# Performance work log

Hardware: AMD Instinct MI355X
Metric: run time of the kernel (lower is better)

Reference implementation:

```python
import jax, jax.numpy as jnp
import numpy as np

B, T, S, C, E, H = 4, 2048, 2048, 256, 512, 8
D = E // H
SCALE = E ** (-0.5)


def setup_inputs() -> dict:
    key = jax.random.key(0)
    ks = jax.random.split(key, 12)
    x = jax.random.normal(ks[0], (B, T, C), dtype=jnp.float32)
    context = jax.random.normal(ks[1], (B, S, E), dtype=jnp.float32)
    pad_mask = jax.random.randint(ks[2], (B, T, S), 0, 2) == 1
    p = 0.02
    # Conv1d kernel_size=1 weights stored squeezed: [out_ch, in_ch]
    w_in = jax.random.normal(ks[3], (E, C), dtype=jnp.float32) * p
    b_in = jnp.zeros((E,), dtype=jnp.float32)
    wq = jax.random.normal(ks[4], (E, E), dtype=jnp.float32) * p
    bq = jnp.zeros((E,), dtype=jnp.float32)
    wk = jax.random.normal(ks[5], (E, E), dtype=jnp.float32) * p
    bk = jnp.zeros((E,), dtype=jnp.float32)
    wv = jax.random.normal(ks[6], (E, E), dtype=jnp.float32) * p
    bv = jnp.zeros((E,), dtype=jnp.float32)
    w_out = jax.random.normal(ks[7], (C, E), dtype=jnp.float32) * p
    b_out = jnp.zeros((C,), dtype=jnp.float32)
    return {"x": x, "context": context, "pad_mask": pad_mask,
            "w_in": w_in, "b_in": b_in, "wq": wq, "bq": bq,
            "wk": wk, "bk": bk, "wv": wv, "bv": bv,
            "w_out": w_out, "b_out": b_out}


def reference(x, context, pad_mask, w_in, b_in, wq, bq, wk, bk, wv, bv, w_out, b_out):
    # proj_in: Conv1d k=1 == per-token linear on channel dim. [B,T,C] -> [B,T,E]
    xe = jnp.einsum('btc,ec->bte', x, w_in) + b_in
    Q = (xe @ wq.T + bq).reshape(B, T, H, D)       # query tokens
    K = (context @ wk.T + bk).reshape(B, S, H, D)  # key tokens
    V = (context @ wv.T + bv).reshape(B, S, H, D)
    att = jnp.einsum('bihd,bjhd->bhij', Q, K) * SCALE  # [B,H,T,S]
    att = jnp.where(pad_mask[:, None, :, :], jnp.float32(-1e9), att)
    att = jax.nn.softmax(att, axis=-1)
    out = jnp.einsum('bhij,bjhd->bihd', att, V).reshape(B, T, E)
    # proj_out: Conv1d k=1, [B,T,E] -> [B,T,C]
    out = jnp.einsum('bte,ce->btc', out, w_out) + b_out
    return out
```

## Files before the change

kernel.cpp:

```cpp
#include <hip/hip_runtime.h>
#include <cstdint>
#include <cstddef>

#define Bb 4
#define Tt 2048
#define Ssz 2048
#define Cc 256
#define Ee 512
#define Hh 8
#define LDK 1024

typedef short bf8 __attribute__((ext_vector_type(8)));
typedef float f4 __attribute__((ext_vector_type(4)));

__device__ __forceinline__ unsigned short f2bf(float x) {
  unsigned int u = __float_as_uint(x);
  u += 0x7fffu + ((u >> 16) & 1u);
  return (unsigned short)(u >> 16);
}

__global__ __launch_bounds__(256) void castk(const float* __restrict__ s,
                                             unsigned short* __restrict__ d,
                                             int n4) {
  int i = blockIdx.x * 256 + threadIdx.x;
  if (i < n4) {
    float4 v = ((const float4*)s)[i];
    ushort4 o;
    o.x = f2bf(v.x);
    o.y = f2bf(v.y);
    o.z = f2bf(v.z);
    o.w = f2bf(v.w);
    ((ushort4*)d)[i] = o;
  }
}

__global__ __launch_bounds__(256) void castw(const float* __restrict__ w0, const float* __restrict__ w1,
                                             const float* __restrict__ w2, const float* __restrict__ w3,
                                             unsigned short* __restrict__ o0, unsigned short* __restrict__ o1,
                                             unsigned short* __restrict__ o2, unsigned short* __restrict__ o3,
                                             float qsc) {
  int i = blockIdx.x * 256 + threadIdx.x;
  const float* s;
  unsigned short* d;
  int off;
  float sc = 1.f;
  if (i < 65536)       { s = w0; d = o0; off = i; sc = qsc; }
  else if (i < 131072) { s = w1; d = o1; off = i - 65536; }
  else if (i < 196608) { s = w2; d = o2; off = i - 131072; }
  else                 { s = w3; d = o3; off = i - 196608; }
  float4 v = ((const float4*)s)[off];
  ushort4 o;
  o.x = f2bf(v.x * sc);
  o.y = f2bf(v.y * sc);
  o.z = f2bf(v.z * sc);
  o.w = f2bf(v.w * sc);
  ((ushort4*)d)[off] = o;
}

__global__ __launch_bounds__(256) void tcast(const float* __restrict__ w,
                                             unsigned short* __restrict__ o) {
  __shared__ float t[64][65];
  const int c0 = blockIdx.x * 64, e0 = blockIdx.y * 64;
  const int tid = threadIdx.x;
  const int row = tid >> 2, c4 = (tid & 3) * 4;
#pragma unroll
  for (int l = 0; l < 4; l++) {
    float4 v = *(const float4*)(w + (size_t)(e0 + row) * Cc + c0 + c4 + l * 16);
    t[row][c4 + l * 16 + 0] = v.x;
    t[row][c4 + l * 16 + 1] = v.y;
    t[row][c4 + l * 16 + 2] = v.z;
    t[row][c4 + l * 16 + 3] = v.w;
  }
  __syncthreads();
#pragma unroll
  for (int l = 0; l < 2; l++) {
    int id = tid + l * 256;
    int c = id >> 3, ch = id & 7;
    bf8 ov;
#pragma unroll
    for (int k = 0; k < 8; k++) {
      int kk = (k + c) & 7;
      ov[kk] = (short)f2bf(t[ch * 8 + kk][c]);
    }
    *(bf8*)(o + (size_t)(c0 + c) * Ee + e0 + ch * 8) = ov;
  }
}

__global__ __launch_bounds__(256) void bqin_k(const float* __restrict__ wq,
                                              const float* __restrict__ b_in,
                                              const float* __restrict__ bq,
                                              float* __restrict__ out, float qsc) {
  int i = blockIdx.x * 256 + threadIdx.x;
  float s = 0.f;
  for (int e = 0; e < Ee; e += 4) {
    float4 w = *(const float4*)(wq + (size_t)i * Ee + e);
    float4 b = *(const float4*)(b_in + e);
    s += w.x * b.x + w.y * b.y + w.z * b.z + w.w * b.w;
  }
  out[i] = (s + bq[i]) * qsc;
}

__global__ __launch_bounds__(256) void packmask(const int* __restrict__ m,
                                                unsigned int* __restrict__ p, int nwords) {
  int i = blockIdx.x * 256 + threadIdx.x;
  if (i >= nwords) return;
  const int4* src = (const int4*)m + (size_t)i * 8;
  unsigned int w = 0;
#pragma unroll
  for (int k = 0; k < 8; k++) {
    int4 v = src[k];
    w |= (unsigned int)(v.x != 0) << (k * 4);
    w |= (unsigned int)(v.y != 0) << (k * 4 + 1);
    w |= (unsigned int)(v.z != 0) << (k * 4 + 2);
    w |= (unsigned int)(v.w != 0) << (k * 4 + 3);
  }
  p[i] = w;
}

__global__ __launch_bounds__(256) void vtrans(const unsigned short* __restrict__ V, int ldv,
                                              unsigned short* __restrict__ Vt) {
  __shared__ unsigned short tile[64][72];
  const int tid = threadIdx.x;
  const int b = blockIdx.z, h = blockIdx.y, s0 = blockIdx.x * 64;
#pragma unroll
  for (int i = 0; i < 2; i++) {
    int id = tid + i * 256;
    int row = id >> 3, c = id & 7;
    *(bf8*)&tile[row][c * 8] =
        *(const bf8*)(V + (size_t)(b * Ssz + s0 + row) * ldv + h * 64 + c * 8);
  }
  __syncthreads();
#pragma unroll
  for (int i = 0; i < 2; i++) {
    int id = tid + i * 256;
    int d = id >> 3, c = id & 7;
    bf8 o;
#pragma unroll
    for (int k = 0; k < 8; k++) {
      int kk = (k + d) & 7;
      o[kk] = (short)tile[c * 8 + kk][d];
    }
    *(bf8*)(Vt + (size_t)((b * Hh + h) * 64 + d) * Ssz + s0 + c * 8) = o;
  }
}

template <bool OUT_BF16, int BM, int BN, int WGM>
__global__ __launch_bounds__(256) void gemm_bt(const unsigned short* __restrict__ A,
                                               const unsigned short* __restrict__ Bt,
                                               const float* __restrict__ bias0,
                                               const float* __restrict__ bias1, int split,
                                               void* __restrict__ Cout,
                                               int M, int N, int K) {
  constexpr int WGN = 4 / WGM;
  constexpr int MI = BM / (WGM * 16);
  constexpr int NJ = BN / (WGN * 16);
  constexpr int NA = BM / 32;
  constexpr int NB = BN / 32;
  __shared__ unsigned short As[BM][72];
  __shared__ unsigned short Bs[BN][72];
  const int tid = threadIdx.x;
  const int wave = tid >> 6, lane = tid & 63;
  const int lrow = lane & 15, quad = lane >> 4;
  const int wm = (wave / WGN) * (BM / WGM);
  const int wn = (wave % WGN) * (BN / WGN);
  const int m0 = blockIdx.x * BM, n0 = blockIdx.y * BN;
  const int arow = tid >> 3, ac = tid & 7;

  f4 acc[MI][NJ];
#pragma unroll
  for (int i = 0; i < MI; i++)
#pragma unroll
    for (int j = 0; j < NJ; j++) {
      f4 z = {0.f, 0.f, 0.f, 0.f};
      acc[i][j] = z;
    }

  bf8 apre[NA], bpre[NB];
#pragma unroll
  for (int i = 0; i < NA; i++)
    apre[i] = *(const bf8*)(A + (size_t)(m0 + arow + i * 32) * K + ac * 8);
#pragma unroll
  for (int i = 0; i < NB; i++)
    bpre[i] = *(const bf8*)(Bt + (size_t)(n0 + arow + i * 32) * K + ac * 8);

  const int nkt = K >> 6;
  for (int kt = 0; kt < nkt; ++kt) {
#pragma unroll
    for (int i = 0; i < NA; i++) *(bf8*)&As[arow + i * 32][ac * 8] = apre[i];
#pragma unroll
    for (int i = 0; i < NB; i++) *(bf8*)&Bs[arow + i * 32][ac * 8] = bpre[i];
    __syncthreads();
    if (kt + 1 < nkt) {
      int k0 = (kt + 1) << 6;
#pragma unroll
      for (int i = 0; i < NA; i++)
        apre[i] = *(const bf8*)(A + (size_t)(m0 + arow + i * 32) * K + k0 + ac * 8);
#pragma unroll
      for (int i = 0; i < NB; i++)
        bpre[i] = *(const bf8*)(Bt + (size_t)(n0 + arow + i * 32) * K + k0 + ac * 8);
    }
#pragma unroll
    for (int kk = 0; kk < 2; kk++) {
      bf8 af[MI], bff[NJ];
#pragma unroll
      for (int i = 0; i < MI; i++)
        af[i] = *(const bf8*)&As[wm + i * 16 + lrow][kk * 32 + quad * 8];
#pragma unroll
      for (int j = 0; j < NJ; j++)
        bff[j] = *(const bf8*)&Bs[wn + j * 16 + lrow][kk * 32 + quad * 8];
#pragma unroll
      for (int i = 0; i < MI; i++)
#pragma unroll
        for (int j = 0; j < NJ; j++)
          acc[i][j] = __builtin_amdgcn_mfma_f32_16x16x32_bf16(af[i], bff[j],
                                                              acc[i][j], 0, 0, 0);
    }
    __syncthreads();
  }

#pragma unroll
  for (int j = 0; j < NJ; j++) {
    int col = n0 + wn + j * 16 + lrow;
    float bvv = 0.f;
    if (bias0) bvv = (col < split) ? bias0[col] : bias1[col - split];
#pragma unroll
    for (int i = 0; i < MI; i++) {
#pragma unroll
      for (int r = 0; r < 4; r++) {
        int row = m0 + wm + i * 16 + quad * 4 + r;
        float v = acc[i][j][r] + bvv;
        if (OUT_BF16)
          ((unsigned short*)Cout)[(size_t)row * N + col] = f2bf(v);
        else
          ((float*)Cout)[(size_t)row * N + col] = v;
      }
    }
  }
}

__global__ __launch_bounds__(256) void attn(const unsigned short* __restrict__ Q,
                                            const unsigned short* __restrict__ K,
                                            const unsigned short* __restrict__ Vt,
                                            const unsigned int* __restrict__ mp,
                                            unsigned short* __restrict__ O) {
  __shared__ unsigned short Ks[64][72];
  __shared__ unsigned short Vts[64][72];
  __shared__ unsigned short Ps[128][72];
  const int tid = threadIdx.x;
  const int wave = tid >> 6, lane = tid & 63;
  const int lrow = lane & 15, quad = lane >> 4;
  const int b = blockIdx.z, h = blockIdx.y, t0 = blockIdx.x * 128;
  const int arow = tid >> 3, ac = tid & 7;
  const int wm = wave * 32;

#pragma unroll
  for (int i = 0; i < 4; i++) {
    int row = arow + i * 32;
    *(bf8*)&Ps[row][ac * 8] =
        *(const bf8*)(Q + (size_t)(b * Tt + t0 + row) * Ee + h * 64 + ac * 8);
  }
  __syncthreads();
  bf8 qf[2][2];
#pragma unroll
  for (int mi = 0; mi < 2; mi++) {
    qf[mi][0] = *(const bf8*)&Ps[wm + mi * 16 + lrow][quad * 8];
    qf[mi][1] = *(const bf8*)&Ps[wm + mi * 16 + lrow][32 + quad * 8];
  }

  f4 oacc[2][4];
  f4 dacc[2];
#pragma unroll
  for (int mi = 0; mi < 2; mi++) {
    f4 z = {0.f, 0.f, 0.f, 0.f};
    dacc[mi] = z;
#pragma unroll
    for (int j = 0; j < 4; j++) oacc[mi][j] = z;
  }
  bf8 ones;
#pragma unroll
  for (int k = 0; k < 8; k++) ones[k] = (short)0x3F80;

  const unsigned short* Kbase = K + (size_t)b * Ssz * LDK + h * 64;
  const unsigned short* Vbase = Vt + (size_t)((b * Hh + h) * 64) * Ssz;

  bf8 kreg[2], vreg[2];
#pragma unroll
  for (int i = 0; i < 2; i++) {
    int row = arow + i * 32;
    kreg[i] = *(const bf8*)(Kbase + (size_t)row * LDK + ac * 8);
    vreg[i] = *(const bf8*)(Vbase + (size_t)row * Ssz + ac * 8);
  }

  for (int s0 = 0; s0 < Ssz; s0 += 64) {
    __syncthreads();
#pragma unroll
    for (int i = 0; i < 2; i++) {
      int row = arow + i * 32;
      *(bf8*)&Ks[row][ac * 8] = kreg[i];
      *(bf8*)&Vts[row][ac * 8] = vreg[i];
    }
    __syncthreads();
    if (s0 + 64 < Ssz) {
#pragma unroll
      for (int i = 0; i < 2; i++) {
        int row = arow + i * 32;
        kreg[i] = *(const bf8*)(Kbase + (size_t)(s0 + 64 + row) * LDK + ac * 8);
        vreg[i] = *(const bf8*)(Vbase + (size_t)row * Ssz + s0 + 64 + ac * 8);
      }
    }
    uint2 mw[2][4];
#pragma unroll
    for (int mi = 0; mi < 2; mi++)
#pragma unroll
      for (int r = 0; r < 4; r++)
        mw[mi][r] = *(const uint2*)(mp + (size_t)(b * Tt + t0 + wm + mi * 16 + quad * 4 + r) * 64 +
                                    (s0 >> 5));

#pragma unroll
    for (int j = 0; j < 4; j++) {
      bf8 kf0 = *(const bf8*)&Ks[j * 16 + lrow][quad * 8];
      bf8 kf1 = *(const bf8*)&Ks[j * 16 + lrow][32 + quad * 8];
      f4 s[2];
      f4 z = {0.f, 0.f, 0.f, 0.f};
      s[0] = z; s[1] = z;
      s[0] = __builtin_amdgcn_mfma_f32_16x16x32_bf16(qf[0][0], kf0, s[0], 0, 0, 0);
      s[0] = __builtin_amdgcn_mfma_f32_16x16x32_bf16(qf[0][1], kf1, s[0], 0, 0, 0);
      s[1] = __builtin_amdgcn_mfma_f32_16x16x32_bf16(qf[1][0], kf0, s[1], 0, 0, 0);
      s[1] = __builtin_amdgcn_mfma_f32_16x16x32_bf16(qf[1][1], kf1, s[1], 0, 0, 0);
      const int col = j * 16 + lrow;
      const unsigned int bit = ((j & 1) << 4) + lrow;
#pragma unroll
      for (int mi = 0; mi < 2; mi++) {
#pragma unroll
        for (int r = 0; r < 4; r++) {
          unsigned int w = (j >> 1) ? mw[mi][r].y : mw[mi][r].x;
          float e = __builtin_amdgcn_exp2f(s[mi][r]);
          float p = ((w >> bit) & 1u) ? 0.f : e;
          Ps[wm + mi * 16 + quad * 4 + r][col] =
              (unsigned short)(__float_as_uint(p) >> 16);
        }
      }
    }
#pragma unroll
    for (int kk = 0; kk < 2; kk++) {
      bf8 pf[2];
#pragma unroll
      for (int mi = 0; mi < 2; mi++) {
        pf[mi] = *(const bf8*)&Ps[wm + mi * 16 + lrow][kk * 32 + quad * 8];
        dacc[mi] = __builtin_amdgcn_mfma_f32_16x16x32_bf16(pf[mi], ones, dacc[mi], 0, 0, 0);
      }
#pragma unroll
      for (int j = 0; j < 4; j++) {
        bf8 vf = *(const bf8*)&Vts[j * 16 + lrow][kk * 32 + quad * 8];
#pragma unroll
        for (int mi = 0; mi < 2; mi++)
          oacc[mi][j] = __builtin_amdgcn_mfma_f32_16x16x32_bf16(pf[mi], vf, oacc[mi][j], 0, 0, 0);
      }
    }
  }

#pragma unroll
  for (int mi = 0; mi < 2; mi++) {
#pragma unroll
    for (int r = 0; r < 4; r++) {
      float inv = 1.0f / dacc[mi][r];
      int row = b * Tt + t0 + wm + mi * 16 + quad * 4 + r;
#pragma unroll
      for (int j = 0; j < 4; j++)
        O[(size_t)row * Ee + h * 64 + j * 16 + lrow] = f2bf(oacc[mi][j][r] * inv);
    }
  }
}

extern "C" void kernel_launch(void* const* d_in, const int* in_sizes, int n_in,
                              void* d_out, int out_size, void* d_ws, size_t ws_size,
                              hipStream_t stream) {
  const float* x    = (const float*)d_in[0];
  const float* ctx  = (const float*)d_in[1];
  const int*   mask = (const int*)d_in[2];
  const float* w_in = (const float*)d_in[3];
  const float* b_in = (const float*)d_in[4];
  const float* wq   = (const float*)d_in[5];
  const float* bq   = (const float*)d_in[6];
  const float* wk   = (const float*)d_in[7];
  const float* bk   = (const float*)d_in[8];
  const float* wv   = (const float*)d_in[9];
  const float* bv   = (const float*)d_in[10];
  const float* wo   = (const float*)d_in[11];
  const float* bo   = (const float*)d_in[12];

  const float qsc = 0.04419417382415922f * 1.4426950408889634f;

  unsigned short* ws = (unsigned short*)d_ws;
  unsigned short* xb   = ws;
  unsigned short* cb   = ws + 2097152;
  unsigned short* wqb  = ws + 6291456;
  unsigned short* wkb  = ws + 6553600;
  unsigned short* wvb  = ws + 6815744;
  unsigned short* wob  = ws + 7077888;
  unsigned short* Qb   = ws + 7208960;
  unsigned short* KVb  = ws + 11403264;
  unsigned short* Ob   = ws + 19791872;
  unsigned short* wqin = Ob;
  unsigned short* winT = Ob + 131072;
  float*          bqinb = (float*)(Ob + 262144);
  unsigned int*   maskp = (unsigned int*)xb;
  unsigned short* Vtb  = cb;

  castk<<<2048, 256, 0, stream>>>(x, xb, 524288);
  castk<<<4096, 256, 0, stream>>>(ctx, cb, 1048576);
  castw<<<896, 256, 0, stream>>>(wq, wk, wv, wo, wqb, wkb, wvb, wob, qsc);
  tcast<<<dim3(4, 8), 256, 0, stream>>>(w_in, winT);
  bqin_k<<<2, 256, 0, stream>>>(wq, b_in, bq, bqinb, qsc);

  gemm_bt<true, 64, 64, 2><<<dim3(8, 4), 256, 0, stream>>>(
      wqb, winT, nullptr, nullptr, 256, wqin, 512, 256, 512);
  gemm_bt<true, 128, 64, 2><<<dim3(64, 8), 256, 0, stream>>>(
      xb, wqin, bqinb, nullptr, 512, Qb, 8192, 512, 256);
  packmask<<<2048, 256, 0, stream>>>(mask, maskp, 524288);
  gemm_bt<true, 128, 128, 2><<<dim3(64, 8), 256, 0, stream>>>(
      cb, wkb, bk, bv, 512, KVb, 8192, 1024, 512);
  vtrans<<<dim3(32, 8, 4), 256, 0, stream>>>(KVb + 512, LDK, Vtb);

  attn<<<dim3(16, 8, 4), 256, 0, stream>>>(Qb, KVb, Vtb, maskp, Ob);

  gemm_bt<false, 64, 64, 2><<<dim3(128, 4), 256, 0, stream>>>(
      Ob, wob, bo, nullptr, 256, d_out, 8192, 256, 512);
}
```

Baseline: 275.2 us.

## Fuse prep kernels, merge mask packing into KV GEMM, double-buffer attention tiles

The separate cast, transpose, bias and weight-product kernels are merged into one multi-role `prep` launch, which now computes wq·w_in straight from fp32 inputs. Mask packing shares a launch with the K/V projection GEMM. The GEMM body is factored into a reusable device function. In attention, K/V shared tiles are double-buffered so one barrier per iteration can be dropped. The score MFMA operands are swapped so each lane's mask word per row is loaded once and P is written as packed ushort4. The aim is fewer launches, fewer barriers and fewer mask loads and LDS stores, at the cost of more shared memory in attention and heterogeneous block roles.

```diff
diff --git a/kernel.cpp b/kernel.cpp
--- a/kernel.cpp
+++ b/kernel.cpp
@@ -19,128 +19,96 @@
   return (unsigned short)(u >> 16);
 }
 
-__global__ __launch_bounds__(256) void castk(const float* __restrict__ s,
-                                             unsigned short* __restrict__ d,
-                                             int n4) {
-  int i = blockIdx.x * 256 + threadIdx.x;
-  if (i < n4) {
-    float4 v = ((const float4*)s)[i];
-    ushort4 o;
-    o.x = f2bf(v.x);
-    o.y = f2bf(v.y);
-    o.z = f2bf(v.z);
-    o.w = f2bf(v.w);
-    ((ushort4*)d)[i] = o;
-  }
-}
-
-__global__ __launch_bounds__(256) void castw(const float* __restrict__ w0, const float* __restrict__ w1,
-                                             const float* __restrict__ w2, const float* __restrict__ w3,
-                                             unsigned short* __restrict__ o0, unsigned short* __restrict__ o1,
-                                             unsigned short* __restrict__ o2, unsigned short* __restrict__ o3,
-                                             float qsc) {
-  int i = blockIdx.x * 256 + threadIdx.x;
-  const float* s;
-  unsigned short* d;
-  int off;
-  float sc = 1.f;
-  if (i < 65536)       { s = w0; d = o0; off = i; sc = qsc; }
-  else if (i < 131072) { s = w1; d = o1; off = i - 65536; }
-  else if (i < 196608) { s = w2; d = o2; off = i - 131072; }
-  else                 { s = w3; d = o3; off = i - 196608; }
-  float4 v = ((const float4*)s)[off];
-  ushort4 o;
-  o.x = f2bf(v.x * sc);
-  o.y = f2bf(v.y * sc);
-  o.z = f2bf(v.z * sc);
-  o.w = f2bf(v.w * sc);
-  ((ushort4*)d)[off] = o;
-}
-
-__global__ __launch_bounds__(256) void tcast(const float* __restrict__ w,
-                                             unsigned short* __restrict__ o) {
-  __shared__ float t[64][65];
-  const int c0 = blockIdx.x * 64, e0 = blockIdx.y * 64;
+template <bool OUT_BF16, int BM, int BN, int WGM>
+__device__ __forceinline__ void gemm_core(unsigned short (*As)[72],
+                                          unsigned short (*Bs)[72],
+                                          const unsigned short* __restrict__ A,
+                                          const unsigned short* __restrict__ Bt,
+                                          const float* __restrict__ bias0,
+                                          const float* __restrict__ bias1, int split,
+                                          void* __restrict__ Cout,
+                                          int M, int N, int K, int m0, int n0) {
+  constexpr int WGN = 4 / WGM;
+  constexpr int MI = BM / (WGM * 16);
+  constexpr int NJ = BN / (WGN * 16);
+  constexpr int NA = BM / 32;
+  constexpr int NB = BN / 32;
   const int tid = threadIdx.x;
-  const int row = tid >> 2, c4 = (tid & 3) * 4;
-#pragma unroll
-  for (int l = 0; l < 4; l++) {
-    float4 v = *(const float4*)(w + (size_t)(e0 + row) * Cc + c0 + c4 + l * 16);
-    t[row][c4 + l * 16 + 0] = v.x;
-    t[row][c4 + l * 16 + 1] = v.y;
-    t[row][c4 + l * 16 + 2] = v.z;
-    t[row][c4 + l * 16 + 3] = v.w;
-  }
-  __syncthreads();
-#pragma unroll
-  for (int l = 0; l < 2; l++) {
-    int id = tid + l * 256;
-    int c = id >> 3, ch = id & 7;
-    bf8 ov;
-#pragma unroll
-    for (int k = 0; k < 8; k++) {
-      int kk = (k + c) & 7;
-      ov[kk] = (short)f2bf(t[ch * 8 + kk][c]);
-    }
-    *(bf8*)(o + (size_t)(c0 + c) * Ee + e0 + ch * 8) = ov;
-  }
-}
-
-__global__ __launch_bounds__(256) void bqin_k(const float* __restrict__ wq,
-                                              const float* __restrict__ b_in,
-                                              const float* __restrict__ bq,
-                                              float* __restrict__ out, float qsc) {
-  int i = blockIdx.x * 256 + threadIdx.x;
-  float s = 0.f;
-  for (int e = 0; e < Ee; e += 4) {
-    float4 w = *(const float4*)(wq + (size_t)i * Ee + e);
-    float4 b = *(const float4*)(b_in + e);
-    s += w.x * b.x + w.y * b.y + w.z * b.z + w.w * b.w;
-  }
-  out[i] = (s + bq[i]) * qsc;
-}
-
-__global__ __launch_bounds__(256) void packmask(const int* __restrict__ m,
-                                                unsigned int* __restrict__ p, int nwords) {
-  int i = blockIdx.x * 256 + threadIdx.x;
-  if (i >= nwords) return;
-  const int4* src = (const int4*)m + (size_t)i * 8;
-  unsigned int w = 0;
-#pragma unroll
-  for (int k = 0; k < 8; k++) {
-    int4 v = src[k];
-    w |= (unsigned int)(v.x != 0) << (k * 4);
-    w |= (unsigned int)(v.y != 0) << (k * 4 + 1);
-    w |= (unsigned int)(v.z != 0) << (k * 4 + 2);
-    w |= (unsigned int)(v.w != 0) << (k * 4 + 3);
-  }
-  p[i] = w;
-}
-
-__global__ __launch_bounds__(256) void vtrans(const unsigned short* __restrict__ V, int ldv,
-                                              unsigned short* __restrict__ Vt) {
-  __shared__ unsigned short tile[64][72];
-  const int tid = threadIdx.x;
-  const int b = blockIdx.z, h = blockIdx.y, s0 = blockIdx.x * 64;
-#pragma unroll
-  for (int i = 0; i < 2; i++) {
-    int id = tid + i * 256;
-    int row = id >> 3, c = id & 7;
-    *(bf8*)&tile[row][c * 8] =
-        *(const bf8*)(V + (size_t)(b * Ssz + s0 + row) * ldv + h * 64 + c * 8);
-  }
-  __syncthreads();
-#pragma unroll
-  for (int i = 0; i < 2; i++) {
-    int id = tid + i * 256;
-    int d = id >> 3, c = id & 7;
-    bf8 o;
-#pragma unroll
-    for (int k = 0; k < 8; k++) {
-      int kk = (k + d) & 7;
-      o[kk] = (short)tile[c * 8 + kk][d];
-    }
-    *(bf8*)(Vt + (size_t)((b * Hh + h) * 64 + d) * Ssz + s0 + c * 8) = o;
+  const int wave = tid >> 6, lane = tid & 63;
+  const int lrow = lane & 15, quad = lane >> 4;
+  const int wm = (wave / WGN) * (BM / WGM);
+  const int wn = (wave % WGN) * (BN / WGN);
+  const int arow = tid >> 3, ac = tid & 7;
+
+  f4 acc[MI][NJ];
+#pragma unroll
+  for (int i = 0; i < MI; i++)
+#pragma unroll
+    for (int j = 0; j < NJ; j++) {
+      f4 z = {0.f, 0.f, 0.f, 0.f};
+      acc[i][j] = z;
+    }
+
+  bf8 apre[NA], bpre[NB];
+#pragma unroll
+  for (int i = 0; i < NA; i++)
+    apre[i] = *(const bf8*)(A + (size_t)(m0 + arow + i * 32) * K + ac * 8);
+#pragma unroll
+  for (int i = 0; i < NB; i++)
+    bpre[i] = *(const bf8*)(Bt + (size_t)(n0 + arow + i * 32) * K + ac * 8);
+
+  const int nkt = K >> 6;
+  for (int kt = 0; kt < nkt; ++kt) {
+#pragma unroll
+    for (int i = 0; i < NA; i++) *(bf8*)&As[arow + i * 32][ac * 8] = apre[i];
+#pragma unroll
+    for (int i = 0; i < NB; i++) *(bf8*)&Bs[arow + i * 32][ac * 8] = bpre[i];
+    __syncthreads();
+    if (kt + 1 < nkt) {
+      int k0 = (kt + 1) << 6;
+#pragma unroll
+      for (int i = 0; i < NA; i++)
+        apre[i] = *(const bf8*)(A + (size_t)(m0 + arow + i * 32) * K + k0 + ac * 8);
+#pragma unroll
+      for (int i = 0; i < NB; i++)
+        bpre[i] = *(const bf8*)(Bt + (size_t)(n0 + arow + i * 32) * K + k0 + ac * 8);
+    }
+#pragma unroll
+    for (int kk = 0; kk < 2; kk++) {
+      bf8 af[MI], bff[NJ];
+#pragma unroll
+      for (int i = 0; i < MI; i++)
+        af[i] = *(const bf8*)&As[wm + i * 16 + lrow][kk * 32 + quad * 8];
+#pragma unroll
+      for (int j = 0; j < NJ; j++)
+        bff[j] = *(const bf8*)&Bs[wn + j * 16 + lrow][kk * 32 + quad * 8];
+#pragma unroll
+      for (int i = 0; i < MI; i++)
+#pragma unroll
+        for (int j = 0; j < NJ; j++)
+          acc[i][j] = __builtin_amdgcn_mfma_f32_16x16x32_bf16(af[i], bff[j],
+                                                              acc[i][j], 0, 0, 0);
+    }
+    __syncthreads();
+  }
+
+#pragma unroll
+  for (int j = 0; j < NJ; j++) {
+    int col = n0 + wn + j * 16 + lrow;
+    float bvv = 0.f;
+    if (bias0) bvv = (col < split) ? bias0[col] : bias1[col - split];
+#pragma unroll
+    for (int i = 0; i < MI; i++) {
+#pragma unroll
+      for (int r = 0; r < 4; r++) {
+        int row = m0 + wm + i * 16 + quad * 4 + r;
+        float v = acc[i][j][r] + bvv;
+        if (OUT_BF16)
+          ((unsigned short*)Cout)[(size_t)row * N + col] = f2bf(v);
+        else
+          ((float*)Cout)[(size_t)row * N + col] = v;
+      }
+    }
   }
 }
 
@@ -151,90 +119,181 @@
                                                const float* __restrict__ bias1, int split,
                                                void* __restrict__ Cout,
                                                int M, int N, int K) {
-  constexpr int WGN = 4 / WGM;
-  constexpr int MI = BM / (WGM * 16);
-  constexpr int NJ = BN / (WGN * 16);
-  constexpr int NA = BM / 32;
-  constexpr int NB = BN / 32;
   __shared__ unsigned short As[BM][72];
   __shared__ unsigned short Bs[BN][72];
+  gemm_core<OUT_BF16, BM, BN, WGM>(As, Bs, A, Bt, bias0, bias1, split, Cout, M, N, K,
+                                   blockIdx.x * BM, blockIdx.y * BN);
+}
+
+__global__ __launch_bounds__(256) void prep(const float* __restrict__ x,
+                                            const float* __restrict__ ctx,
+                                            const float* __restrict__ w_in,
+                                            const float* __restrict__ b_in,
+                                            const float* __restrict__ wq,
+                                            const float* __restrict__ bq,
+                                            const float* __restrict__ wk,
+                                            const float* __restrict__ wv,
+                                            const float* __restrict__ wo,
+                                            unsigned short* __restrict__ xb,
+                                            unsigned short* __restrict__ cb,
+                                            unsigned short* __restrict__ wkvb,
+                                            unsigned short* __restrict__ wob,
+                                            unsigned short* __restrict__ wqin,
+                                            float* __restrict__ bqinb, float qsc) {
+  __shared__ unsigned short sh[128][72];
+  const int bid = blockIdx.x, tid = threadIdx.x;
+  if (bid < 6144) {
+    const float* s;
+    unsigned short* d;
+    int i;
+    if (bid < 2048) { s = x; d = xb; i = bid * 256 + tid; }
+    else            { s = ctx; d = cb; i = (bid - 2048) * 256 + tid; }
+    float4 v = ((const float4*)s)[i];
+    ushort4 o;
+    o.x = f2bf(v.x); o.y = f2bf(v.y); o.z = f2bf(v.z); o.w = f2bf(v.w);
+    ((ushort4*)d)[i] = o;
+  } else if (bid < 6784) {
+    int i = (bid - 6144) * 256 + tid;
+    const float* s;
+    unsigned short* d;
+    int off;
+    if (i < 131072)      { s = wk; d = wkvb; off = i; }
+    else                 { s = wo; d = wob; off = i - 131072; }
+    if (i >= 65536 && i < 131072) { s = wv; off = i - 65536; d = wkvb + 262144; }
+    float4 v = ((const float4*)s)[off];
+    ushort4 o;
+    o.x = f2bf(v.x); o.y = f2bf(v.y); o.z = f2bf(v.z); o.w = f2bf(v.w);
+    ((ushort4*)d)[off] = o;
+  } else if (bid < 6816) {
+    const int idx = bid - 6784;
+    const int m0 = (idx & 7) * 64, n0 = (idx >> 3) * 64;
+    unsigned short (*As)[72] = (unsigned short (*)[72]) & sh[0][0];
+    unsigned short (*Bs)[72] = (unsigned short (*)[72]) & sh[64][0];
+    const int wave = tid >> 6, lane = tid & 63;
+    const int lrow = lane & 15, quad = lane >> 4;
+    const int wm = (wave >> 1) * 32, wn = (wave & 1) * 32;
+    const int arow = tid >> 3, ac = tid & 7;
+    f4 acc[2][2];
+#pragma unroll
+    for (int i = 0; i < 2; i++)
+#pragma unroll
+      for (int j = 0; j < 2; j++) {
+        f4 z = {0.f, 0.f, 0.f, 0.f};
+        acc[i][j] = z;
+      }
+    for (int kt = 0; kt < 8; kt++) {
+#pragma unroll
+      for (int i = 0; i < 2; i++) {
+        int row = arow + i * 32;
+        const float* src = wq + (size_t)(m0 + row) * Ee + kt * 64 + ac * 8;
+        float4 v0 = *(const float4*)src, v1 = *(const float4*)(src + 4);
+        bf8 av;
+        av[0] = (short)f2bf(v0.x * qsc); av[1] = (short)f2bf(v0.y * qsc);
+        av[2] = (short)f2bf(v0.z * qsc); av[3] = (short)f2bf(v0.w * qsc);
+        av[4] = (short)f2bf(v1.x * qsc); av[5] = (short)f2bf(v1.y * qsc);
+        av[6] = (short)f2bf(v1.z * qsc); av[7] = (short)f2bf(v1.w * qsc);
+        *(bf8*)&As[row][ac * 8] = av;
+        int c = n0 + row;
+        bf8 bv;
+#pragma unroll
+        for (int k = 0; k < 8; k++)
+          bv[k] = (short)f2bf(w_in[(size_t)(kt * 64 + ac * 8 + k) * Cc + c]);
+        *(bf8*)&Bs[row][ac * 8] = bv;
+      }
+      __syncthreads();
+#pragma unroll
+      for (int kk = 0; kk < 2; kk++) {
+        bf8 af[2], bff[2];
+#pragma unroll
+        for (int i = 0; i < 2; i++) af[i] = *(const bf8*)&As[wm + i * 16 + lrow][kk * 32 + quad * 8];
+#pragma unroll
+        for (int j = 0; j < 2; j++) bff[j] = *(const bf8*)&Bs[wn + j * 16 + lrow][kk * 32 + quad * 8];
+#pragma unroll
+        for (int i = 0; i < 2; i++)
+#pragma unroll
+          for (int j = 0; j < 2; j++)
+            acc[i][j] = __builtin_amdgcn_mfma_f32_16x16x32_bf16(af[i], bff[j], acc[i][j], 0, 0, 0);
+      }
+      __syncthreads();
+    }
+#pragma unroll
+    for (int j = 0; j < 2; j++)
+#pragma unroll
+      for (int i = 0; i < 2; i++)
+#pragma unroll
+        for (int r = 0; r < 4; r++)
+          wqin[(size_t)(m0 + wm + i * 16 + quad * 4 + r) * Cc + n0 + wn + j * 16 + lrow] =
+              f2bf(acc[i][j][r]);
+  } else {
+    const int o = (bid - 6816) * 32 + (tid >> 3);
+    const int k0 = (tid & 7) * 64;
+    float s = 0.f;
+#pragma unroll
+    for (int i = 0; i < 16; i++) {
+      float4 w = *(const float4*)(wq + (size_t)o * Ee + k0 + i * 4);
+      float4 bb = *(const float4*)(b_in + k0 + i * 4);
+      s += w.x * bb.x + w.y * bb.y + w.z * bb.z + w.w * bb.w;
+    }
+    s += __shfl_xor(s, 1);
+    s += __shfl_xor(s, 2);
+    s += __shfl_xor(s, 4);
+    if ((tid & 7) == 0) bqinb[o] = (s + bq[o]) * qsc;
+  }
+}
+
+__global__ __launch_bounds__(256) void kvpack(const unsigned short* __restrict__ cb,
+                                              const unsigned short* __restrict__ wkv,
+                                              const float* __restrict__ bk,
+                                              const float* __restrict__ bv,
+                                              unsigned short* __restrict__ KVout,
+                                              const int* __restrict__ mask,
+                                              unsigned int* __restrict__ mp) {
+  __shared__ unsigned short As[128][72];
+  __shared__ unsigned short Bs[128][72];
+  const int bid = blockIdx.x;
+  if (bid < 512) {
+    gemm_core<true, 128, 128, 2>(As, Bs, cb, wkv, bk, bv, 512, KVout, 8192, 1024, 512,
+                                 (bid & 63) * 128, (bid >> 6) * 128);
+  } else {
+    int i = (bid - 512) * 256 + threadIdx.x;
+    const int4* src = (const int4*)mask + (size_t)i * 8;
+    unsigned int w = 0;
+#pragma unroll
+    for (int k = 0; k < 8; k++) {
+      int4 v = src[k];
+      w |= (unsigned int)(v.x != 0) << (k * 4);
+      w |= (unsigned int)(v.y != 0) << (k * 4 + 1);
+      w |= (unsigned int)(v.z != 0) << (k * 4 + 2);
+      w |= (unsigned int)(v.w != 0) << (k * 4 + 3);
+    }
+    mp[i] = w;
+  }
+}
+
+__global__ __launch_bounds__(256) void vtrans(const unsigned short* __restrict__ V, int ldv,
+                                              unsigned short* __restrict__ Vt) {
+  __shared__ unsigned short tile[64][72];
   const int tid = threadIdx.x;
-  const int wave = tid >> 6, lane = tid & 63;
-  const int lrow = lane & 15, quad = lane >> 4;
-  const int wm = (wave / WGN) * (BM / WGM);
-  const int wn = (wave % WGN) * (BN / WGN);
-  const int m0 = blockIdx.x * BM, n0 = blockIdx.y * BN;
-  const int arow = tid >> 3, ac = tid & 7;
-
-  f4 acc[MI][NJ];
-#pragma unroll
-  for (int i = 0; i < MI; i++)
-#pragma unroll
-    for (int j = 0; j < NJ; j++) {
-      f4 z = {0.f, 0.f, 0.f, 0.f};
-      acc[i][j] = z;
-    }
-
-  bf8 apre[NA], bpre[NB];
-#pragma unroll
-  for (int i = 0; i < NA; i++)
-    apre[i] = *(const bf8*)(A + (size_t)(m0 + arow + i * 32) * K + ac * 8);
-#pragma unroll
-  for (int i = 0; i < NB; i++)
-    bpre[i] = *(const bf8*)(Bt + (size_t)(n0 + arow + i * 32) * K + ac * 8);
-
-  const int nkt = K >> 6;
-  for (int kt = 0; kt < nkt; ++kt) {
-#pragma unroll
-    for (int i = 0; i < NA; i++) *(bf8*)&As[arow + i * 32][ac * 8] = apre[i];
-#pragma unroll
-    for (int i = 0; i < NB; i++) *(bf8*)&Bs[arow + i * 32][ac * 8] = bpre[i];
-    __syncthreads();
-    if (kt + 1 < nkt) {
-      int k0 = (kt + 1) << 6;
-#pragma unroll
-      for (int i = 0; i < NA; i++)
-        apre[i] = *(const bf8*)(A + (size_t)(m0 + arow + i * 32) * K + k0 + ac * 8);
-#pragma unroll
-      for (int i = 0; i < NB; i++)
-        bpre[i] = *(const bf8*)(Bt + (size_t)(n0 + arow + i * 32) * K + k0 + ac * 8);
-    }
-#pragma unroll
-    for (int kk = 0; kk < 2; kk++) {
-      bf8 af[MI], bff[NJ];
-#pragma unroll
-      for (int i = 0; i < MI; i++)
-        af[i] = *(const bf8*)&As[wm + i * 16 + lrow][kk * 32 + quad * 8];
-#pragma unroll
-      for (int j = 0; j < NJ; j++)
-        bff[j] = *(const bf8*)&Bs[wn + j * 16 + lrow][kk * 32 + quad * 8];
-#pragma unroll
-      for (int i = 0; i < MI; i++)
-#pragma unroll
-        for (int j = 0; j < NJ; j++)
-          acc[i][j] = __builtin_amdgcn_mfma_f32_16x16x32_bf16(af[i], bff[j],
-                                                              acc[i][j], 0, 0, 0);
-    }
-    __syncthreads();
-  }
-
-#pragma unroll
-  for (int j = 0; j < NJ; j++) {
-    int col = n0 + wn + j * 16 + lrow;
-    float bvv = 0.f;
-    if (bias0) bvv = (col < split) ? bias0[col] : bias1[col - split];
-#pragma unroll
-    for (int i = 0; i < MI; i++) {
-#pragma unroll
-      for (int r = 0; r < 4; r++) {
-        int row = m0 + wm + i * 16 + quad * 4 + r;
-        float v = acc[i][j][r] + bvv;
-        if (OUT_BF16)
-          ((unsigned short*)Cout)[(size_t)row * N + col] = f2bf(v);
-        else
-          ((float*)Cout)[(size_t)row * N + col] = v;
-      }
-    }
+  const int b = blockIdx.z, h = blockIdx.y, s0 = blockIdx.x * 64;
+#pragma unroll
+  for (int i = 0; i < 2; i++) {
+    int id = tid + i * 256;
+    int row = id >> 3, c = id & 7;
+    *(bf8*)&tile[row][c * 8] =
+        *(const bf8*)(V + (size_t)(b * Ssz + s0 + row) * ldv + h * 64 + c * 8);
+  }
+  __syncthreads();
+#pragma unroll
+  for (int i = 0; i < 2; i++) {
+    int id = tid + i * 256;
+    int d = id >> 3, c = id & 7;
+    bf8 o;
+#pragma unroll
+    for (int k = 0; k < 8; k++) {
+      int kk = (k + d) & 7;
+      o[kk] = (short)tile[c * 8 + kk][d];
+    }
+    *(bf8*)(Vt + (size_t)((b * Hh + h) * 64 + d) * Ssz + s0 + c * 8) = o;
   }
 }
 
@@ -243,8 +302,8 @@
                                             const unsigned short* __restrict__ Vt,
                                             const unsigned int* __restrict__ mp,
                                             unsigned short* __restrict__ O) {
-  __shared__ unsigned short Ks[64][72];
-  __shared__ unsigned short Vts[64][72];
+  __shared__ unsigned short Ks[2][64][72];
+  __shared__ unsigned short Vts[2][64][72];
   __shared__ unsigned short Ps[128][72];
   const int tid = threadIdx.x;
   const int wave = tid >> 6, lane = tid & 63;
@@ -282,6 +341,8 @@
 
   const unsigned short* Kbase = K + (size_t)b * Ssz * LDK + h * 64;
   const unsigned short* Vbase = Vt + (size_t)((b * Hh + h) * 64) * Ssz;
+  const unsigned int* mrow0 = mp + (size_t)(b * Tt + t0 + wm + lrow) * 64;
+  const unsigned int* mrow1 = mp + (size_t)(b * Tt + t0 + wm + 16 + lrow) * 64;
 
   bf8 kreg[2], vreg[2];
 #pragma unroll
@@ -291,13 +352,13 @@
     vreg[i] = *(const bf8*)(Vbase + (size_t)row * Ssz + ac * 8);
   }
 
+  int buf = 0;
   for (int s0 = 0; s0 < Ssz; s0 += 64) {
-    __syncthreads();
 #pragma unroll
     for (int i = 0; i < 2; i++) {
       int row = arow + i * 32;
-      *(bf8*)&Ks[row][ac * 8] = kreg[i];
-      *(bf8*)&Vts[row][ac * 8] = vreg[i];
+      *(bf8*)&Ks[buf][row][ac * 8] = kreg[i];
+      *(bf8*)&Vts[buf][row][ac * 8] = vreg[i];
     }
     __syncthreads();
     if (s0 + 64 < Ssz) {
@@ -308,37 +369,37 @@
         vreg[i] = *(const bf8*)(Vbase + (size_t)row * Ssz + s0 + 64 + ac * 8);
       }
     }
-    uint2 mw[2][4];
-#pragma unroll
-    for (int mi = 0; mi < 2; mi++)
-#pragma unroll
-      for (int r = 0; r < 4; r++)
-        mw[mi][r] = *(const uint2*)(mp + (size_t)(b * Tt + t0 + wm + mi * 16 + quad * 4 + r) * 64 +
-                                    (s0 >> 5));
-
-#pragma unroll
-    for (int j = 0; j < 4; j++) {
-      bf8 kf0 = *(const bf8*)&Ks[j * 16 + lrow][quad * 8];
-      bf8 kf1 = *(const bf8*)&Ks[j * 16 + lrow][32 + quad * 8];
-      f4 s[2];
+    const uint2 mw0 = *(const uint2*)(mrow0 + (s0 >> 5));
+    const uint2 mw1 = *(const uint2*)(mrow1 + (s0 >> 5));
+
+#pragma unroll
+    for (int sf = 0; sf < 4; sf++) {
+      bf8 kf0 = *(const bf8*)&Ks[buf][sf * 16 + lrow][quad * 8];
+      bf8 kf1 = *(const bf8*)&Ks[buf][sf * 16 + lrow][32 + quad * 8];
+      f4 sa[2];
       f4 z = {0.f, 0.f, 0.f, 0.f};
-      s[0] = z; s[1] = z;
-      s[0] = __builtin_amdgcn_mfma_f32_16x16x32_bf16(qf[0][0], kf0, s[0], 0, 0, 0);
-      s[0] = __builtin_amdgcn_mfma_f32_16x16x32_bf16(qf[0][1], kf1, s[0], 0, 0, 0);
-      s[1] = __builtin_amdgcn_mfma_f32_16x16x32_bf16(qf[1][0], kf0, s[1], 0, 0, 0);
-      s[1] = __builtin_amdgcn_mfma_f32_16x16x32_bf16(qf[1][1], kf1, s[1], 0, 0, 0);
-      const int col = j * 16 + lrow;
-      const unsigned int bit = ((j & 1) << 4) + lrow;
+      sa[0] = z; sa[1] = z;
+      sa[0] = __builtin_amdgcn_mfma_f32_16x16x32_bf16(kf0, qf[0][0], sa[0], 0, 0, 0);
+      sa[0] = __builtin_amdgcn_mfma_f32_16x16x32_bf16(kf1, qf[0][1], sa[0], 0, 0, 0);
+      sa[1] = __builtin_amdgcn_mfma_f32_16x16x32_bf16(kf0, qf[1][0], sa[1], 0, 0, 0);
+      sa[1] = __builtin_amdgcn_mfma_f32_16x16x32_bf16(kf1, qf[1][1], sa[1], 0, 0, 0);
 #pragma unroll
       for (int mi = 0; mi < 2; mi++) {
+        const uint2 mw = mi ? mw1 : mw0;
+        const unsigned int w = (sf >= 2) ? mw.y : mw.x;
+        ushort4 pk;
 #pragma unroll
         for (int r = 0; r < 4; r++) {
-          unsigned int w = (j >> 1) ? mw[mi][r].y : mw[mi][r].x;
-          float e = __builtin_amdgcn_exp2f(s[mi][r]);
+          const unsigned int bit = (sf & 1) * 16 + quad * 4 + r;
+          float e = __builtin_amdgcn_exp2f(sa[mi][r]);
           float p = ((w >> bit) & 1u) ? 0.f : e;
-          Ps[wm + mi * 16 + quad * 4 + r][col] =
-              (unsigned short)(__float_as_uint(p) >> 16);
+          unsigned short pb = (unsigned short)(__float_as_uint(p) >> 16);
+          if (r == 0) pk.x = pb;
+          else if (r == 1) pk.y = pb;
+          else if (r == 2) pk.z = pb;
+          else pk.w = pb;
         }
+        *(ushort4*)&Ps[wm + mi * 16 + lrow][sf * 16 + quad * 4] = pk;
       }
     }
 #pragma unroll
@@ -351,12 +412,13 @@
       }
 #pragma unroll
       for (int j = 0; j < 4; j++) {
-        bf8 vf = *(const bf8*)&Vts[j * 16 + lrow][kk * 32 + quad * 8];
+        bf8 vf = *(const bf8*)&Vts[buf][j * 16 + lrow][kk * 32 + quad * 8];
 #pragma unroll
         for (int mi = 0; mi < 2; mi++)
           oacc[mi][j] = __builtin_amdgcn_mfma_f32_16x16x32_bf16(pf[mi], vf, oacc[mi][j], 0, 0, 0);
       }
     }
+    buf ^= 1;
   }
 
 #pragma unroll
@@ -392,38 +454,25 @@
   const float qsc = 0.04419417382415922f * 1.4426950408889634f;
 
   unsigned short* ws = (unsigned short*)d_ws;
-  unsigned short* xb   = ws;
-  unsigned short* cb   = ws + 2097152;
-  unsigned short* wqb  = ws + 6291456;
-  unsigned short* wkb  = ws + 6553600;
-  unsigned short* wvb  = ws + 6815744;
-  unsigned short* wob  = ws + 7077888;
-  unsigned short* Qb   = ws + 7208960;
-  unsigned short* KVb  = ws + 11403264;
-  unsigned short* Ob   = ws + 19791872;
-  unsigned short* wqin = Ob;
-  unsigned short* winT = Ob + 131072;
-  float*          bqinb = (float*)(Ob + 262144);
+  unsigned short* xb    = ws;
+  unsigned short* cb    = ws + 2097152;
+  unsigned short* wkvb  = ws + 6291456;
+  unsigned short* wob   = ws + 6815744;
+  unsigned short* wqin  = ws + 6946816;
+  float*          bqinb = (float*)(ws + 7077888);
+  unsigned short* Qb    = ws + 7208960;
+  unsigned short* KVb   = ws + 11403264;
+  unsigned short* Ob    = ws + 19791872;
   unsigned int*   maskp = (unsigned int*)xb;
-  unsigned short* Vtb  = cb;
-
-  castk<<<2048, 256, 0, stream>>>(x, xb, 524288);
-  castk<<<4096, 256, 0, stream>>>(ctx, cb, 1048576);
-  castw<<<896, 256, 0, stream>>>(wq, wk, wv, wo, wqb, wkb, wvb, wob, qsc);
-  tcast<<<dim3(4, 8), 256, 0, stream>>>(w_in, winT);
-  bqin_k<<<2, 256, 0, stream>>>(wq, b_in, bq, bqinb, qsc);
-
-  gemm_bt<true, 64, 64, 2><<<dim3(8, 4), 256, 0, stream>>>(
-      wqb, winT, nullptr, nullptr, 256, wqin, 512, 256, 512);
+  unsigned short* Vtb   = cb;
+
+  prep<<<6832, 256, 0, stream>>>(x, ctx, w_in, b_in, wq, bq, wk, wv, wo,
+                                 xb, cb, wkvb, wob, wqin, bqinb, qsc);
   gemm_bt<true, 128, 64, 2><<<dim3(64, 8), 256, 0, stream>>>(
       xb, wqin, bqinb, nullptr, 512, Qb, 8192, 512, 256);
-  packmask<<<2048, 256, 0, stream>>>(mask, maskp, 524288);
-  gemm_bt<true, 128, 128, 2><<<dim3(64, 8), 256, 0, stream>>>(
-      cb, wkb, bk, bv, 512, KVb, 8192, 1024, 512);
+  kvpack<<<2560, 256, 0, stream>>>(cb, wkvb, bk, bv, KVb, mask, maskp);
   vtrans<<<dim3(32, 8, 4), 256, 0, stream>>>(KVb + 512, LDK, Vtb);
-
   attn<<<dim3(16, 8, 4), 256, 0, stream>>>(Qb, KVb, Vtb, maskp, Ob);
-
   gemm_bt<false, 64, 64, 2><<<dim3(128, 4), 256, 0, stream>>>(
       Ob, wob, bo, nullptr, 256, d_out, 8192, 256, 512);
 }
```

Result: faster. 252.6 us (-8.2%).
